# Optimization experiments

Hardware: AMD Instinct MI355X
Metric: run time of the kernel (lower is better)

Reference implementation:

```python
import jax, jax.numpy as jnp
import numpy as np

BATCH = 4
N1 = 131072   # stage-1 voxels (total over batch)
N2 = 32768    # stage-2 (stride-2 downsampled) voxels
D_MODEL = 128
D_INNER = 2 * D_MODEL
D_STATE = 16
D_CONV = 4
DT_RANK = 8   # ceil(d_model / 16)
EPS = 1e-5


def _ln(x, g, b):
    mu = x.mean(-1, keepdims=True)
    v = ((x - mu) ** 2).mean(-1, keepdims=True)
    return (x - mu) * jax.lax.rsqrt(v + EPS) * g + b


def _causal_conv(x, w, b):
    # x: [B,L,Di], w: [Di,K] -> depthwise causal conv1d
    y = jax.lax.conv_general_dilated(
        x.transpose(0, 2, 1), w[:, None, :], (1,), [(D_CONV - 1, 0)],
        dimension_numbers=('NCH', 'OIH', 'NCH'), feature_group_count=D_INNER)
    return y.transpose(0, 2, 1) + b


def _mamba_block(x, ln_g, ln_b, in_w, conv_w, conv_b, xproj_w, dtproj_w, dtproj_b, A_log, Dp, out_w):
    # create_block: LayerNorm -> Mamba mixer (selective scan); returns hidden states
    h = _ln(x, ln_g, ln_b)
    xz = h @ in_w.T                          # [B,L,2*Di]
    xc, z = jnp.split(xz, 2, axis=-1)
    xc = jax.nn.silu(_causal_conv(xc, conv_w, conv_b))
    dbl = xc @ xproj_w.T                     # [B,L,dt_rank+2*d_state]
    dt = jax.nn.softplus(dbl[..., :DT_RANK] @ dtproj_w.T + dtproj_b)  # [B,L,Di]
    Bm = dbl[..., DT_RANK:DT_RANK + D_STATE]
    Cm = dbl[..., DT_RANK + D_STATE:]
    A = -jnp.exp(A_log)                      # [Di,ds]

    def step(hst, inp):
        dt_t, b_t, c_t, u_t = inp            # [B,Di],[B,ds],[B,ds],[B,Di]
        hst = jnp.exp(dt_t[..., None] * A) * hst + (dt_t * u_t)[..., None] * b_t[:, None, :]
        return hst, jnp.einsum('bds,bs->bd', hst, c_t)

    h0 = jnp.zeros((x.shape[0], D_INNER, D_STATE), x.dtype)
    xs = (dt.transpose(1, 0, 2), Bm.transpose(1, 0, 2), Cm.transpose(1, 0, 2), xc.transpose(1, 0, 2))
    _, ys = jax.lax.scan(step, h0, xs)       # ys: [L,B,Di]
    y = ys.transpose(1, 0, 2) + xc * Dp
    y = y * jax.nn.silu(z)
    return y @ out_w.T


def _mamba_params(key):
    ks = jax.random.split(key, 6)
    s = lambda k, sh, sc: jax.random.normal(k, sh, jnp.float32) * sc
    return dict(
        ln_g=jnp.ones((D_MODEL,), jnp.float32), ln_b=jnp.zeros((D_MODEL,), jnp.float32),
        in_w=s(ks[0], (2 * D_INNER, D_MODEL), 0.05),
        conv_w=s(ks[1], (D_INNER, D_CONV), 0.2), conv_b=jnp.zeros((D_INNER,), jnp.float32),
        xproj_w=s(ks[2], (DT_RANK + 2 * D_STATE, D_INNER), 0.05),
        dtproj_w=s(ks[3], (D_INNER, DT_RANK), 0.1), dtproj_b=s(ks[4], (D_INNER,), 0.1),
        A_log=jnp.log(jnp.tile(jnp.arange(1, D_STATE + 1, dtype=jnp.float32), (D_INNER, 1))),
        D=jnp.ones((D_INNER,), jnp.float32),
        out_w=s(ks[5], (D_MODEL, D_INNER), 0.05))


def setup_inputs():
    key = jax.random.key(0)
    k = jax.random.split(key, 10)
    inp = {
        'feats_s1': jax.random.normal(k[0], (N1, D_MODEL), jnp.float32),
        'feats_s2': jax.random.normal(k[1], (N2, D_MODEL), jnp.float32),
        'pos_s1': jax.random.uniform(k[2], (N1, 3), jnp.float32),
        'pos_s2': jax.random.uniform(k[3], (N2, 3), jnp.float32),
        'hilbert_s1': jax.random.randint(k[4], (N1,), 0, 1 << 30, jnp.int32),
        'hilbert_s2': jax.random.randint(k[5], (N2,), 0, 1 << 30, jnp.int32),
        'pe_w': jax.random.normal(k[6], (D_MODEL, 3), jnp.float32) * 0.1,
        'pe_b': jnp.zeros((D_MODEL,), jnp.float32),
        'norm_g': jnp.ones((D_MODEL,), jnp.float32), 'norm_b': jnp.zeros((D_MODEL,), jnp.float32),
        'normb_g': jnp.ones((D_MODEL,), jnp.float32), 'normb_b': jnp.zeros((D_MODEL,), jnp.float32),
    }
    for pref, kk in (('m1_', k[7]), ('m2_', k[8])):
        for n, v in _mamba_params(kk).items():
            inp[pref + n] = v
    return inp


def _forward(feats_s1, feats_s2, pos_s1, pos_s2, pe_w, pe_b, norm_g, norm_b, normb_g, normb_b,
             m1_ln_g, m1_ln_b, m1_in_w, m1_conv_w, m1_conv_b, m1_xproj_w, m1_dtproj_w, m1_dtproj_b, m1_A_log, m1_D, m1_out_w,
             m2_ln_g, m2_ln_b, m2_in_w, m2_conv_w, m2_conv_b, m2_xproj_w, m2_dtproj_w, m2_dtproj_b, m2_A_log, m2_D, m2_out_w,
             hilbert_s1, hilbert_s2):
    L1, L2 = N1 // BATCH, N2 // BATCH
    m1 = (m1_ln_g, m1_ln_b, m1_in_w, m1_conv_w, m1_conv_b, m1_xproj_w, m1_dtproj_w, m1_dtproj_b, m1_A_log, m1_D, m1_out_w)
    m2 = (m2_ln_g, m2_ln_b, m2_in_w, m2_conv_w, m2_conv_b, m2_xproj_w, m2_dtproj_w, m2_dtproj_b, m2_A_log, m2_D, m2_out_w)

    # stage 2: hilbert-order forward scan through mamba_layer1
    f2 = (feats_s2 + pos_s2 @ pe_w.T + pe_b).reshape(BATCH, L2, D_MODEL)
    o2 = jnp.argsort(hilbert_s2.reshape(BATCH, L2), axis=-1)          # inds_curt_to_next
    seq2 = jnp.take_along_axis(f2, o2[..., None], axis=1)
    out2 = _mamba_block(seq2, *m1)
    back2 = jnp.take_along_axis(out2, jnp.argsort(o2, axis=-1)[..., None], axis=1).reshape(N2, D_MODEL)
    out_s2 = _ln(back2, norm_g, norm_b)

    # stage 1: flipped hilbert-order (backward) scan through mamba_layer2
    f1 = (feats_s1 + pos_s1 @ pe_w.T + pe_b).reshape(BATCH, L1, D_MODEL)
    o1 = jnp.argsort(hilbert_s1.reshape(BATCH, L1), axis=-1)
    seq1 = jnp.take_along_axis(f1, o1[..., None], axis=1)[:, ::-1, :]
    out1 = _mamba_block(seq1, *m2)[:, ::-1, :]
    back1 = jnp.take_along_axis(out1, jnp.argsort(o1, axis=-1)[..., None], axis=1).reshape(N1, D_MODEL)
    out_s1 = _ln(back1, normb_g, normb_b)

    return jnp.concatenate([out_s1, out_s2], axis=0)   # [N1+N2, d_model]


def reference(feats_s1, feats_s2, pos_s1, pos_s2, pe_w, pe_b, norm_g, norm_b, normb_g, normb_b,
              m1_ln_g, m1_ln_b, m1_in_w, m1_conv_w, m1_conv_b, m1_xproj_w, m1_dtproj_w, m1_dtproj_b, m1_A_log, m1_D, m1_out_w,
              m2_ln_g, m2_ln_b, m2_in_w, m2_conv_w, m2_conv_b, m2_xproj_w, m2_dtproj_w, m2_dtproj_b, m2_A_log, m2_D, m2_out_w,
              hilbert_s1, hilbert_s2):
    return _forward(feats_s1, feats_s2, pos_s1, pos_s2, pe_w, pe_b, norm_g, norm_b, normb_g, normb_b,
                    m1_ln_g, m1_ln_b, m1_in_w, m1_conv_w, m1_conv_b, m1_xproj_w, m1_dtproj_w, m1_dtproj_b, m1_A_log, m1_D, m1_out_w,
                    m2_ln_g, m2_ln_b, m2_in_w, m2_conv_w, m2_conv_b, m2_xproj_w, m2_dtproj_w, m2_dtproj_b, m2_A_log, m2_D, m2_out_w,
                    hilbert_s1, hilbert_s2)
```

## Files before the change

### kernel.cpp

```cpp
#include <hip/hip_runtime.h>
#include <hip/hip_bf16.h>

#define DEV __device__ __forceinline__

constexpr int BATCH_ = 4;
constexpr int N1_ = 131072;
constexpr int N2_ = 32768;
constexpr int L1_ = N1_ / BATCH_;
constexpr int L2_ = N2_ / BATCH_;
constexpr int DM_ = 128;
constexpr int DI_ = 256;
constexpr int DS_ = 16;
constexpr int DTR_ = 8;
constexpr int TOT_ = N1_ + N2_;

constexpr int TA_ = 32;
constexpr int TAH_ = TA_ + 3;
constexpr int NTILE1_ = L1_ / TA_;
constexpr int NTILE2_ = L2_ / TA_;
constexpr int NTILES_ = 4 * NTILE1_ + 4 * NTILE2_;

constexpr int TS_ = 128;
constexpr int NCH1_ = L1_ / TS_;
constexpr int NCH2_ = L2_ / TS_;
constexpr int NCHUNKS_ = 4 * NCH1_ + 4 * NCH2_;

constexpr int NST_ = 160;

constexpr int PADR_ = 16;
constexpr int SR1_ = L1_ + 2 * PADR_;
constexpr int SR2_ = L2_ + 2 * PADR_;
constexpr int RTOT_ = 4 * SR1_ + 4 * SR2_;

constexpr int IN1_OFF = 0;
constexpr int IN2_OFF = 65536;
constexpr int XP1_OFF = 131072;
constexpr int XP2_OFF = 143360;
constexpr int OW1_OFF = 155648;
constexpr int OW2_OFF = 188416;
constexpr int W16_TOT = 221184;

typedef short short8 __attribute__((ext_vector_type(8)));
typedef float f32x4 __attribute__((ext_vector_type(4)));

struct MP {
  const float* ln_g; const float* ln_b; const float* in_w;
  const float* conv_w; const float* conv_b; const float* xproj_w;
  const float* dtproj_w; const float* dtproj_b; const float* A_log;
  const float* Dp; const float* out_w;
};

DEV float softplusf(float x) {
  return fmaxf(x, 0.f) + __logf(1.f + __expf(-fabsf(x)));
}

DEV unsigned short f2bf(float f) {
  unsigned u = __builtin_bit_cast(unsigned, f);
  u += 0x7fffu + ((u >> 16) & 1u);
  return (unsigned short)(u >> 16);
}
DEV float bf2f(unsigned short s) {
  unsigned u = ((unsigned)s) << 16;
  return __builtin_bit_cast(float, u);
}

DEV void sort_tile_info(int tile, int& seg, int& tis, int& slotbase) {
  if (tile < 128) { seg = tile >> 5; tis = tile & 31; slotbase = seg * L1_; }
  else { seg = 4 + ((tile - 128) >> 3); tis = (tile - 128) & 7; slotbase = N1_ + (seg - 4) * L2_; }
}

__global__ __launch_bounds__(256) void k_prep(
    const float* __restrict__ in_w1, const float* __restrict__ xp1,
    const float* __restrict__ ow1,
    const float* __restrict__ in_w2, const float* __restrict__ xp2,
    const float* __restrict__ ow2,
    unsigned short* __restrict__ w16)
{
  const int i = blockIdx.x * 256 + threadIdx.x;
  if (i >= W16_TOT) return;
  float v;
  if (i < IN2_OFF) v = in_w1[i - IN1_OFF];
  else if (i < XP1_OFF) v = in_w2[i - IN2_OFF];
  else if (i < XP2_OFF) {
    const int j = i - XP1_OFF; const int r = j >> 8;
    v = (r < 40) ? xp1[j] : 0.f;
  } else if (i < OW1_OFF) {
    const int j = i - XP2_OFF; const int r = j >> 8;
    v = (r < 40) ? xp2[j] : 0.f;
  } else if (i < OW2_OFF) v = ow1[i - OW1_OFF];
  else v = ow2[i - OW2_OFF];
  w16[i] = f2bf(v);
}

__global__ __launch_bounds__(256) void k_hist(
    const int* __restrict__ hil1, const int* __restrict__ hil2,
    const unsigned* __restrict__ ksrc, unsigned* __restrict__ histg,
    int shift, int pass0)
{
  const int tile = blockIdx.x;
  int seg, tis, slotbase;
  sort_tile_info(tile, seg, tis, slotbase);
  const int tid = threadIdx.x;
  __shared__ unsigned h[1024];
  #pragma unroll
  for (int i = 0; i < 4; ++i) h[i * 256 + tid] = 0;
  __syncthreads();
  #pragma unroll
  for (int it = 0; it < 4; ++it) {
    const int li = tis * 1024 + it * 256 + tid;
    unsigned k;
    if (pass0) k = (unsigned)(seg < 4 ? hil1[seg * L1_ + li] : hil2[(seg - 4) * L2_ + li]);
    else       k = ksrc[slotbase + li];
    atomicAdd(&h[(k >> shift) & 1023u], 1u);
  }
  __syncthreads();
  #pragma unroll
  for (int i = 0; i < 4; ++i)
    histg[tile * 1024 + i * 256 + tid] = h[i * 256 + tid];
}

__global__ __launch_bounds__(256) void k_scanoff(
    const unsigned* __restrict__ histg, unsigned* __restrict__ offg)
{
  const int seg = blockIdx.x;
  const int ntiles = seg < 4 ? 32 : 8;
  const int tilebase = seg < 4 ? seg * 32 : 128 + (seg - 4) * 8;
  const int tid = threadIdx.x;
  const int d0 = tid * 4;
  unsigned tot[4] = {0, 0, 0, 0};
  for (int t = 0; t < ntiles; ++t) {
    const unsigned* hp = &histg[(size_t)(tilebase + t) * 1024 + d0];
    tot[0] += hp[0]; tot[1] += hp[1]; tot[2] += hp[2]; tot[3] += hp[3];
  }
  unsigned lp[4]; unsigned s = 0;
  #pragma unroll
  for (int j = 0; j < 4; ++j) { lp[j] = s; s += tot[j]; }
  const int lane = tid & 63, wv = tid >> 6;
  unsigned inc = s;
  #pragma unroll
  for (int off = 1; off < 64; off <<= 1) {
    unsigned v = (unsigned)__shfl_up((int)inc, off, 64);
    if (lane >= off) inc += v;
  }
  __shared__ unsigned wsum[4];
  if (lane == 63) wsum[wv] = inc;
  __syncthreads();
  unsigned wbase = 0;
  for (int w = 0; w < 4; ++w) if (w < wv) wbase += wsum[w];
  const unsigned base = wbase + inc - s;
  #pragma unroll
  for (int j = 0; j < 4; ++j) {
    unsigned run = base + lp[j];
    for (int t = 0; t < ntiles; ++t) {
      offg[(size_t)(tilebase + t) * 1024 + d0 + j] = run;
      run += histg[(size_t)(tilebase + t) * 1024 + d0 + j];
    }
  }
}

__global__ __launch_bounds__(256) void k_scatter(
    const int* __restrict__ hil1, const int* __restrict__ hil2,
    const unsigned* __restrict__ ksrc, const int* __restrict__ isrc,
    const unsigned* __restrict__ offg,
    unsigned* __restrict__ kdst, int* __restrict__ idst,
    int* __restrict__ o_all, int shift, int pass0, int last)
{
  const int tile = blockIdx.x;
  int seg, tis, slotbase;
  sort_tile_info(tile, seg, tis, slotbase);
  const int tid = threadIdx.x;
  const int lane = tid & 63, wv = tid >> 6;
  __shared__ unsigned runb[1024];
  __shared__ unsigned wcnt[4 * 1024];
  #pragma unroll
  for (int i = 0; i < 4; ++i) runb[i * 256 + tid] = offg[(size_t)tile * 1024 + i * 256 + tid];
  #pragma unroll
  for (int it = 0; it < 4; ++it) {
    #pragma unroll
    for (int i = 0; i < 16; ++i) wcnt[i * 256 + tid] = 0;
    __syncthreads();
    const int li = tis * 1024 + it * 256 + tid;
    unsigned k; int v;
    if (pass0) {
      k = (unsigned)(seg < 4 ? hil1[seg * L1_ + li] : hil2[(seg - 4) * L2_ + li]);
      v = li;
    } else {
      k = ksrc[slotbase + li]; v = isrc[slotbase + li];
    }
    const unsigned d = (k >> shift) & 1023u;
    unsigned long long m = ~0ull;
    #pragma unroll
    for (int b = 0; b < 10; ++b) {
      const unsigned long long bb = __ballot((int)((d >> b) & 1u));
      m &= ((d >> b) & 1u) ? bb : ~bb;
    }
    const unsigned lrank = (unsigned)__popcll(m & ((1ull << lane) - 1ull));
    wcnt[wv * 1024 + d] = (unsigned)__popcll(m);
    __syncthreads();
    unsigned prior = runb[d];
    for (int w = 0; w < 3; ++w) if (w < wv) prior += wcnt[w * 1024 + d];
    const unsigned pos = prior + lrank;
    if (last) o_all[slotbase + pos] = v;
    else { kdst[slotbase + pos] = k; idst[slotbase + pos] = v; }
    __syncthreads();
    #pragma unroll
    for (int i = 0; i < 4; ++i) {
      const int dd = i * 256 + tid;
      runb[dd] += wcnt[dd] + wcnt[1024 + dd] + wcnt[2048 + dd] + wcnt[3072 + dd];
    }
    __syncthreads();
  }
}

__global__ __launch_bounds__(256) void k_gather(
    const float* __restrict__ feats1, const float* __restrict__ feats2,
    const float* __restrict__ pos1, const float* __restrict__ pos2,
    const float* __restrict__ pe_w, const float* __restrict__ pe_b,
    MP p1, MP p2, const int* __restrict__ o_all,
    unsigned* __restrict__ seq_g)
{
  const int wv = threadIdx.x >> 6, lane = threadIdx.x & 63;
  const int prow = blockIdx.x * 4 + wv;
  if (prow >= RTOT_) return;
  int seg, within;
  if (prow < 4 * SR1_) { seg = prow / SR1_; within = prow - seg * SR1_; }
  else { const int r = prow - 4 * SR1_; seg = 4 + r / SR2_; within = r - (seg - 4) * SR2_; }
  const bool is1 = seg < 4;
  const int b = is1 ? seg : seg - 4;
  const int L = is1 ? L1_ : L2_;
  const int p = within - PADR_;
  unsigned outw = 0;
  if (p >= 0 && p < L) {
    const int slotbase = is1 ? b * L1_ : N1_ + b * L2_;
    const int orig = o_all[slotbase + p];
    const MP P = is1 ? p2 : p1;
    const float* fr = (is1 ? feats1 + (size_t)b * L1_ * DM_
                           : feats2 + (size_t)b * L2_ * DM_) + (size_t)orig * DM_;
    const float* pr = (is1 ? pos1 + (size_t)b * L1_ * 3
                           : pos2 + (size_t)b * L2_ * 3) + (size_t)orig * 3;
    const int c0 = 2 * lane;
    const float2 f = *(const float2*)(fr + c0);
    const float q0 = pr[0], q1 = pr[1], q2 = pr[2];
    float x0 = f.x + q0 * pe_w[c0 * 3 + 0] + q1 * pe_w[c0 * 3 + 1] + q2 * pe_w[c0 * 3 + 2] + pe_b[c0];
    float x1 = f.y + q0 * pe_w[c0 * 3 + 3] + q1 * pe_w[c0 * 3 + 4] + q2 * pe_w[c0 * 3 + 5] + pe_b[c0 + 1];
    float s = x0 + x1, qq = x0 * x0 + x1 * x1;
    #pragma unroll
    for (int off = 32; off; off >>= 1) {
      s += __shfl_xor(s, off, 64);
      qq += __shfl_xor(qq, off, 64);
    }
    const float mu = s * (1.f / 128.f);
    const float rs = rsqrtf(qq * (1.f / 128.f) - mu * mu + 1e-5f);
    const unsigned short o0 = f2bf((x0 - mu) * rs * P.ln_g[c0]     + P.ln_b[c0]);
    const unsigned short o1 = f2bf((x1 - mu) * rs * P.ln_g[c0 + 1] + P.ln_b[c0 + 1]);
    outw = (unsigned)o0 | ((unsigned)o1 << 16);
  }
  seq_g[(size_t)prow * 64 + lane] = outw;
}

constexpr int XB_ = 264;
constexpr int SMEM_A = TAH_ * XB_ * 2;

__global__ __launch_bounds__(256) void k_phaseA(
    MP p1, MP p2,
    const unsigned short* __restrict__ seq_g,
    const unsigned short* __restrict__ w16,
    __hip_bfloat16* __restrict__ xc_g, __hip_bfloat16* __restrict__ z_g,
    float* __restrict__ dbl_g)
{
  const int blk = blockIdx.x;
  bool is1; int b, tile;
  if (blk < 4 * NTILE1_) { is1 = true; b = blk / NTILE1_; tile = blk % NTILE1_; }
  else { const int r = blk - 4 * NTILE1_; is1 = false; b = r / NTILE2_; tile = r % NTILE2_; }
  const int slotbase = is1 ? b * L1_ : N1_ + b * L2_;
  const MP P = is1 ? p2 : p1;
  const unsigned short* iw16 = w16 + (is1 ? IN2_OFF : IN1_OFF);
  const unsigned short* xp16 = w16 + (is1 ? XP2_OFF : XP1_OFF);
  const int segrow0 = is1 ? b * SR1_ : 4 * SR1_ + b * SR2_;
  const unsigned short* seq = seq_g + (size_t)segrow0 * DM_;
  const bool rev = is1;
  const int t0 = tile * TA_;
  const int pstart = rev ? t0 : t0 - 3;
  const int lsh = rev ? 0 : 3;

  __shared__ char smem[SMEM_A];
  unsigned short* xcb16 = (unsigned short*)smem;
  unsigned short* xc16 = xcb16;

  const int tid = threadIdx.x;
  const int lane = tid & 63, wv = tid >> 6;
  const int l15 = lane & 15, quad = lane >> 4;

  #pragma unroll
  for (int mt = 0; mt < 3; ++mt) {
    const int arow = PADR_ + pstart + mt * 16 + l15;
    short8 afr[4];
    #pragma unroll
    for (int t = 0; t < 4; ++t)
      afr[t] = *(const short8*)(seq + (size_t)arow * DM_ + t * 32 + quad * 8);
    #pragma unroll
    for (int nn2 = 0; nn2 < 4; ++nn2) {
      const int ntA = nn2 * 8 + wv;
      const int ntB = nn2 * 8 + 4 + wv;
      f32x4 accA = (f32x4){0.f, 0.f, 0.f, 0.f}, accB = accA;
      #pragma unroll
      for (int t = 0; t < 4; ++t) {
        const short8 bfA = *(const short8*)(iw16 + (size_t)(ntA * 16 + l15) * DM_ + t * 32 + quad * 8);
        const short8 bfB = *(const short8*)(iw16 + (size_t)(ntB * 16 + l15) * DM_ + t * 32 + quad * 8);
        accA = __builtin_amdgcn_mfma_f32_16x16x32_bf16(afr[t], bfA, accA, 0, 0, 0);
        accB = __builtin_amdgcn_mfma_f32_16x16x32_bf16(afr[t], bfB, accB, 0, 0, 0);
      }
      const int row0 = mt * 16 + quad * 4;
      const int colA = ntA * 16 + l15;
      const int colB = ntB * 16 + l15;
      #pragma unroll
      for (int r = 0; r < 4; ++r) {
        const int row = row0 + r;
        if (colA < 256) {
          if (row < TAH_) xcb16[row * XB_ + colA] = f2bf(accA[r]);
        } else {
          const int m = row - lsh;
          if (m >= 0 && m < TA_)
            z_g[(size_t)(slotbase + t0 + m) * DI_ + (colA - 256)] = __float2bfloat16(accA[r]);
        }
        if (colB < 256) {
          if (row < TAH_) xcb16[row * XB_ + colB] = f2bf(accB[r]);
        } else {
          const int m = row - lsh;
          if (m >= 0 && m < TA_)
            z_g[(size_t)(slotbase + t0 + m) * DI_ + (colB - 256)] = __float2bfloat16(accB[r]);
        }
      }
    }
  }
  __syncthreads();
  {
    const int d = tid;
    const float w0 = P.conv_w[d * 4 + 0], w1 = P.conv_w[d * 4 + 1],
                w2 = P.conv_w[d * 4 + 2], w3 = P.conv_w[d * 4 + 3];
    const float cb = P.conv_b[d];
    float x0 = bf2f(xcb16[0 * XB_ + d]), x1 = bf2f(xcb16[1 * XB_ + d]),
          x2 = bf2f(xcb16[2 * XB_ + d]);
    #pragma unroll
    for (int m = 0; m < TA_; ++m) {
      const float x3 = bf2f(xcb16[(m + 3) * XB_ + d]);
      float v;
      if (rev) v = w3 * x0 + w2 * x1 + w1 * x2 + w0 * x3;
      else     v = w0 * x0 + w1 * x1 + w2 * x2 + w3 * x3;
      v += cb;
      v = v * (1.f / (1.f + __expf(-v)));
      const unsigned short vb = f2bf(v);
      xc_g[(size_t)(slotbase + t0 + m) * DI_ + d] = __builtin_bit_cast(__hip_bfloat16, vb);
      xcb16[m * XB_ + d] = vb;
      x0 = x1; x1 = x2; x2 = x3;
    }
  }
  __syncthreads();
  if (wv < 3) {
    f32x4 acc0 = (f32x4){0.f,0.f,0.f,0.f}, acc1 = acc0;
    #pragma unroll
    for (int t = 0; t < 8; ++t) {
      const short8 bfr = *(const short8*)(xp16 + (size_t)(wv * 16 + l15) * DI_ + t * 32 + quad * 8);
      const short8 a0 = *(const short8*)(xc16 + (l15) * XB_ + t * 32 + quad * 8);
      const short8 a1 = *(const short8*)(xc16 + (16 + l15) * XB_ + t * 32 + quad * 8);
      acc0 = __builtin_amdgcn_mfma_f32_16x16x32_bf16(a0, bfr, acc0, 0, 0, 0);
      acc1 = __builtin_amdgcn_mfma_f32_16x16x32_bf16(a1, bfr, acc1, 0, 0, 0);
    }
    const int col = wv * 16 + l15;
    if (col < 40) {
      #pragma unroll
      for (int r = 0; r < 4; ++r) {
        dbl_g[(size_t)(slotbase + t0 + quad * 4 + r) * 40 + col] = acc0[r];
        dbl_g[(size_t)(slotbase + t0 + 16 + quad * 4 + r) * 40 + col] = acc1[r];
      }
    }
  }
}

struct ScanP {
  float Av[DS_]; float A0; bool fast;
  float dtw[DTR_]; float dtb;
};
DEV void load_scanp(const MP& P, int d, ScanP& sp) {
  #pragma unroll
  for (int s = 0; s < DS_; ++s) sp.Av[s] = -__expf(P.A_log[d * DS_ + s]);
  sp.A0 = sp.Av[0];
  bool f = true;
  #pragma unroll
  for (int s = 0; s < DS_; ++s)
    f = f && (fabsf(sp.Av[s] - (float)(s + 1) * sp.A0) <= 1e-3f * (float)(s + 1));
  sp.fast = f;
  #pragma unroll
  for (int r = 0; r < DTR_; ++r) sp.dtw[r] = P.dtproj_w[d * DTR_ + r];
  sp.dtb = P.dtproj_b[d];
}
DEV float dt_from(const float4& q0, const float4& q1, const ScanP& sp) {
  const float dtraw = sp.dtb
      + q0.x*sp.dtw[0] + q0.y*sp.dtw[1] + q0.z*sp.dtw[2] + q0.w*sp.dtw[3]
      + q1.x*sp.dtw[4] + q1.y*sp.dtw[5] + q1.z*sp.dtw[6] + q1.w*sp.dtw[7];
  return softplusf(dtraw);
}

__global__ __launch_bounds__(256) void k_scan1(
    MP p1, MP p2,
    const __hip_bfloat16* __restrict__ xc_g, const float* __restrict__ dbl_g,
    float* __restrict__ hloc, float* __restrict__ sumdt_g)
{
  const int blk = blockIdx.x;
  bool is1; int b, pc;
  if (blk < 4 * NCH1_) { is1 = true; b = blk / NCH1_; pc = blk % NCH1_; }
  else { const int r = blk - 4 * NCH1_; is1 = false; b = r / NCH2_; pc = r % NCH2_; }
  const MP P = is1 ? p2 : p1;
  const int L = is1 ? L1_ : L2_;
  const bool rev = is1;
  const int slotbase = is1 ? b * L1_ : N1_ + b * L2_;
  const int d = threadIdx.x;
  ScanP sp; load_scanp(P, d, sp);
  const unsigned short* xcp = (const unsigned short*)xc_g;
  float h[DS_];
  #pragma unroll
  for (int s = 0; s < DS_; ++s) h[s] = 0.f;
  float sdt = 0.f;
  const int s0 = rev ? (L - (pc + 1) * TS_) : pc * TS_;
  const int dp = rev ? -1 : 1;
  int slot = slotbase + (rev ? (s0 + TS_ - 1) : s0);
  if (sp.fast) {
    const float* dr = dbl_g + (size_t)slot * 40;
    float4 q0 = *(const float4*)dr, q1 = *(const float4*)(dr + 4);
    float4 Bv[4];
    #pragma unroll
    for (int j = 0; j < 4; ++j) Bv[j] = *(const float4*)(dr + 8 + 4 * j);
    float u = bf2f(xcp[(size_t)slot * DI_ + d]);
    for (int i = 0; i < TS_; ++i) {
      const int nslot = (i + 1 < TS_) ? slot + dp : slot;
      const float* nr = dbl_g + (size_t)nslot * 40;
      float4 nq0 = *(const float4*)nr, nq1 = *(const float4*)(nr + 4);
      float4 nB[4];
      #pragma unroll
      for (int j = 0; j < 4; ++j) nB[j] = *(const float4*)(nr + 8 + 4 * j);
      const float nu = bf2f(xcp[(size_t)nslot * DI_ + d]);
      const float dt = dt_from(q0, q1, sp);
      const float du = dt * u;
      sdt += dt;
      const float e1 = __expf(dt * sp.A0);
      const float e2 = e1 * e1, e3 = e2 * e1, e4 = e2 * e2;
      float base = 1.f;
      #pragma unroll
      for (int j = 0; j < 4; ++j) {
        const float m1 = base * e1, m2 = base * e2, m3 = base * e3, m4 = base * e4;
        h[4*j+0] = m1 * h[4*j+0] + du * Bv[j].x;
        h[4*j+1] = m2 * h[4*j+1] + du * Bv[j].y;
        h[4*j+2] = m3 * h[4*j+2] + du * Bv[j].z;
        h[4*j+3] = m4 * h[4*j+3] + du * Bv[j].w;
        base = m4;
      }
      slot = nslot; q0 = nq0; q1 = nq1; u = nu;
      #pragma unroll
      for (int j = 0; j < 4; ++j) Bv[j] = nB[j];
    }
  } else {
    for (int i = 0; i < TS_; ++i) {
      const float* dr = dbl_g + (size_t)slot * 40;
      const float4 q0 = *(const float4*)dr, q1 = *(const float4*)(dr + 4);
      const float dt = dt_from(q0, q1, sp);
      const float u = bf2f(xcp[(size_t)slot * DI_ + d]);
      const float du = dt * u;
      sdt += dt;
      float Bvv[16];
      #pragma unroll
      for (int j = 0; j < 4; ++j) *(float4*)&Bvv[4*j] = *(const float4*)(dr + 8 + 4*j);
      #pragma unroll
      for (int s = 0; s < DS_; ++s)
        h[s] = __expf(dt * sp.Av[s]) * h[s] + du * Bvv[s];
      slot += dp;
    }
  }
  float* hl = hloc + (size_t)blk * DS_ * DI_;
  #pragma unroll
  for (int s = 0; s < DS_; ++s) hl[s * DI_ + d] = h[s];
  sumdt_g[(size_t)blk * DI_ + d] = sdt;
}

__global__ __launch_bounds__(256) void k_scan2(
    MP p1, MP p2, const float* __restrict__ hloc,
    const float* __restrict__ sumdt_g, float* __restrict__ hin)
{
  const int seq = blockIdx.x >> 4;
  const int s = blockIdx.x & 15;
  const bool is1 = seq < 4;
  const int b = is1 ? seq : seq - 4;
  const MP P = is1 ? p2 : p1;
  const int nch = is1 ? NCH1_ : NCH2_;
  const int chbase = is1 ? b * NCH1_ : 4 * NCH1_ + b * NCH2_;
  const int d = threadIdx.x;
  const float A = -__expf(P.A_log[d * DS_ + s]);
  float carry = 0.f;
  for (int pc = 0; pc < nch; ++pc) {
    const size_t idx = (size_t)(chbase + pc);
    const float sdt = sumdt_g[idx * DI_ + d];
    hin[idx * DS_ * DI_ + s * DI_ + d] = carry;
    carry = __expf(A * sdt) * carry + hloc[idx * DS_ * DI_ + s * DI_ + d];
  }
}

__global__ __launch_bounds__(256) void k_scan3(
    MP p1, MP p2,
    const __hip_bfloat16* __restrict__ xc_g, const float* __restrict__ dbl_g,
    const float* __restrict__ hin, __hip_bfloat16* zv_g)
{
  const int blk = blockIdx.x;
  bool is1; int b, pc;
  if (blk < 4 * NCH1_) { is1 = true; b = blk / NCH1_; pc = blk % NCH1_; }
  else { const int r = blk - 4 * NCH1_; is1 = false; b = r / NCH2_; pc = r % NCH2_; }
  const MP P = is1 ? p2 : p1;
  const int L = is1 ? L1_ : L2_;
  const bool rev = is1;
  const int slotbase = is1 ? b * L1_ : N1_ + b * L2_;
  const int d = threadIdx.x;
  ScanP sp; load_scanp(P, d, sp);
  const float Dp = P.Dp[d];
  const unsigned short* xcp = (const unsigned short*)xc_g;
  unsigned short* zvp = (unsigned short*)zv_g;
  float h[DS_];
  const float* hi = hin + (size_t)blk * DS_ * DI_;
  #pragma unroll
  for (int s = 0; s < DS_; ++s) h[s] = hi[s * DI_ + d];
  const int s0 = rev ? (L - (pc + 1) * TS_) : pc * TS_;
  const int dp = rev ? -1 : 1;
  int slot = slotbase + (rev ? (s0 + TS_ - 1) : s0);
  if (sp.fast) {
    const float* dr = dbl_g + (size_t)slot * 40;
    float4 q0 = *(const float4*)dr, q1 = *(const float4*)(dr + 4);
    float4 Bv[4], Cv[4];
    #pragma unroll
    for (int j = 0; j < 4; ++j) {
      Bv[j] = *(const float4*)(dr + 8 + 4 * j);
      Cv[j] = *(const float4*)(dr + 24 + 4 * j);
    }
    float u = bf2f(xcp[(size_t)slot * DI_ + d]);
    float zv = bf2f(zvp[(size_t)slot * DI_ + d]);
    for (int i = 0; i < TS_; ++i) {
      const int nslot = (i + 1 < TS_) ? slot + dp : slot;
      const float* nr = dbl_g + (size_t)nslot * 40;
      float4 nq0 = *(const float4*)nr, nq1 = *(const float4*)(nr + 4);
      float4 nB[4], nC[4];
      #pragma unroll
      for (int j = 0; j < 4; ++j) {
        nB[j] = *(const float4*)(nr + 8 + 4 * j);
        nC[j] = *(const float4*)(nr + 24 + 4 * j);
      }
      const float nu = bf2f(xcp[(size_t)nslot * DI_ + d]);
      const float nz = bf2f(zvp[(size_t)nslot * DI_ + d]);
      const float dt = dt_from(q0, q1, sp);
      const float du = dt * u;
      const float e1 = __expf(dt * sp.A0);
      const float e2 = e1 * e1, e3 = e2 * e1, e4 = e2 * e2;
      float base = 1.f;
      float y = 0.f;
      #pragma unroll
      for (int j = 0; j < 4; ++j) {
        const float m1 = base * e1, m2 = base * e2, m3 = base * e3, m4 = base * e4;
        h[4*j+0] = m1 * h[4*j+0] + du * Bv[j].x;  y += h[4*j+0] * Cv[j].x;
        h[4*j+1] = m2 * h[4*j+1] + du * Bv[j].y;  y += h[4*j+1] * Cv[j].y;
        h[4*j+2] = m3 * h[4*j+2] + du * Bv[j].z;  y += h[4*j+2] * Cv[j].z;
        h[4*j+3] = m4 * h[4*j+3] + du * Bv[j].w;  y += h[4*j+3] * Cv[j].w;
        base = m4;
      }
      const float sg = zv / (1.f + __expf(-zv));
      zvp[(size_t)slot * DI_ + d] = f2bf((y + u * Dp) * sg);
      slot = nslot; q0 = nq0; q1 = nq1; u = nu; zv = nz;
      #pragma unroll
      for (int j = 0; j < 4; ++j) { Bv[j] = nB[j]; Cv[j] = nC[j]; }
    }
  } else {
    for (int i = 0; i < TS_; ++i) {
      const float* dr = dbl_g + (size_t)slot * 40;
      const float4 q0 = *(const float4*)dr, q1 = *(const float4*)(dr + 4);
      const float dt = dt_from(q0, q1, sp);
      const float u = bf2f(xcp[(size_t)slot * DI_ + d]);
      const float zv = bf2f(zvp[(size_t)slot * DI_ + d]);
      const float du = dt * u;
      float Bvv[16], Cvv[16];
      #pragma unroll
      for (int j = 0; j < 4; ++j) {
        *(float4*)&Bvv[4*j] = *(const float4*)(dr + 8 + 4*j);
        *(float4*)&Cvv[4*j] = *(const float4*)(dr + 24 + 4*j);
      }
      float y = 0.f;
      #pragma unroll
      for (int s = 0; s < DS_; ++s) {
        h[s] = __expf(dt * sp.Av[s]) * h[s] + du * Bvv[s];
        y += h[s] * Cvv[s];
      }
      const float sg = zv / (1.f + __expf(-zv));
      zvp[(size_t)slot * DI_ + d] = f2bf((y + u * Dp) * sg);
      slot += dp;
    }
  }
}

constexpr int OB_ = 132;
__global__ __launch_bounds__(256) void k_final(
    const __hip_bfloat16* __restrict__ v_g, const int* __restrict__ o_all,
    const unsigned short* __restrict__ w16,
    const float* __restrict__ norm_g, const float* __restrict__ norm_b,
    const float* __restrict__ normb_g, const float* __restrict__ normb_b,
    float* __restrict__ out)
{
  const int blk = blockIdx.x;
  bool is1; int b, tile;
  if (blk < 4 * NTILE1_) { is1 = true; b = blk / NTILE1_; tile = blk % NTILE1_; }
  else { const int r = blk - 4 * NTILE1_; is1 = false; b = r / NTILE2_; tile = r % NTILE2_; }
  const unsigned short* W = w16 + (is1 ? OW2_OFF : OW1_OFF);
  const float* gg = is1 ? normb_g : norm_g;
  const float* gb = is1 ? normb_b : norm_b;
  const int slotbase = is1 ? b * L1_ : N1_ + b * L2_;
  const int t0 = tile * TA_;
  __shared__ float obuf[TA_ * OB_];
  const int tid = threadIdx.x;
  const int lane = tid & 63, wv = tid >> 6;
  const int l15 = lane & 15, quad = lane >> 4;
  {
    const unsigned short* vp = (const unsigned short*)v_g + (size_t)(slotbase + t0) * DI_;
    f32x4 acc00 = (f32x4){0.f,0.f,0.f,0.f}, acc01 = acc00, acc10 = acc00, acc11 = acc00;
    #pragma unroll
    for (int t = 0; t < 8; ++t) {
      const short8 a0 = *(const short8*)(vp + (size_t)(l15) * DI_ + t * 32 + quad * 8);
      const short8 a1 = *(const short8*)(vp + (size_t)(16 + l15) * DI_ + t * 32 + quad * 8);
      const short8 b0 = *(const short8*)(W + (size_t)((wv) * 16 + l15) * DI_ + t * 32 + quad * 8);
      const short8 b1 = *(const short8*)(W + (size_t)((wv + 4) * 16 + l15) * DI_ + t * 32 + quad * 8);
      acc00 = __builtin_amdgcn_mfma_f32_16x16x32_bf16(a0, b0, acc00, 0, 0, 0);
      acc01 = __builtin_amdgcn_mfma_f32_16x16x32_bf16(a1, b0, acc01, 0, 0, 0);
      acc10 = __builtin_amdgcn_mfma_f32_16x16x32_bf16(a0, b1, acc10, 0, 0, 0);
      acc11 = __builtin_amdgcn_mfma_f32_16x16x32_bf16(a1, b1, acc11, 0, 0, 0);
    }
    const int col0 = wv * 16 + l15;
    const int col1 = (wv + 4) * 16 + l15;
    #pragma unroll
    for (int r = 0; r < 4; ++r) {
      obuf[(quad * 4 + r) * OB_ + col0] = acc00[r];
      obuf[(16 + quad * 4 + r) * OB_ + col0] = acc01[r];
      obuf[(quad * 4 + r) * OB_ + col1] = acc10[r];
      obuf[(16 + quad * 4 + r) * OB_ + col1] = acc11[r];
    }
  }
  __syncthreads();
  {
    for (int m = wv; m < TA_; m += 4) {
      float x0 = obuf[m * OB_ + lane], x1 = obuf[m * OB_ + lane + 64];
      float s = x0 + x1, q = x0 * x0 + x1 * x1;
      #pragma unroll
      for (int off = 32; off; off >>= 1) {
        s += __shfl_xor(s, off, 64);
        q += __shfl_xor(q, off, 64);
      }
      const float mu = s * (1.f / 128.f);
      const float rs = rsqrtf(q * (1.f / 128.f) - mu * mu + 1e-5f);
      const int orig = o_all[slotbase + t0 + m];
      float* orow = out + (size_t)(slotbase + orig) * DM_;
      orow[lane]      = (x0 - mu) * rs * gg[lane]      + gb[lane];
      orow[lane + 64] = (x1 - mu) * rs * gg[lane + 64] + gb[lane + 64];
    }
  }
}

extern "C" void kernel_launch(void* const* d_in, const int* in_sizes, int n_in,
                              void* d_out, int out_size, void* d_ws, size_t ws_size,
                              hipStream_t stream)
{
  (void)in_sizes; (void)n_in; (void)out_size; (void)ws_size;
  const float* feats1 = (const float*)d_in[0];
  const float* feats2 = (const float*)d_in[1];
  const float* pos1   = (const float*)d_in[2];
  const float* pos2   = (const float*)d_in[3];
  const int*   hil1   = (const int*)d_in[4];
  const int*   hil2   = (const int*)d_in[5];
  const float* pe_w   = (const float*)d_in[6];
  const float* pe_b   = (const float*)d_in[7];
  const float* norm_g  = (const float*)d_in[8];
  const float* norm_b  = (const float*)d_in[9];
  const float* normb_g = (const float*)d_in[10];
  const float* normb_b = (const float*)d_in[11];
  MP p1 { (const float*)d_in[12], (const float*)d_in[13], (const float*)d_in[14],
          (const float*)d_in[15], (const float*)d_in[16], (const float*)d_in[17],
          (const float*)d_in[18], (const float*)d_in[19], (const float*)d_in[20],
          (const float*)d_in[21], (const float*)d_in[22] };
  MP p2 { (const float*)d_in[23], (const float*)d_in[24], (const float*)d_in[25],
          (const float*)d_in[26], (const float*)d_in[27], (const float*)d_in[28],
          (const float*)d_in[29], (const float*)d_in[30], (const float*)d_in[31],
          (const float*)d_in[32], (const float*)d_in[33] };

  char* w = (char*)d_ws;
  auto take = [&](size_t bytes) -> char* {
    char* p = w; w += (bytes + 255) & ~(size_t)255; return p;
  };
  int* o_all = (int*)take((size_t)TOT_ * 4);
  unsigned* kA = (unsigned*)take((size_t)TOT_ * 4);
  int* iA = (int*)take((size_t)TOT_ * 4);
  unsigned* kB = (unsigned*)take((size_t)TOT_ * 4);
  int* iB = (int*)take((size_t)TOT_ * 4);
  unsigned* histg = (unsigned*)take((size_t)NST_ * 1024 * 4);
  unsigned* offg  = (unsigned*)take((size_t)NST_ * 1024 * 4);
  __hip_bfloat16* xc = (__hip_bfloat16*)take((size_t)TOT_ * DI_ * 2);
  __hip_bfloat16* vzb = (__hip_bfloat16*)take((size_t)TOT_ * DI_ * 2);
  float* dbl = (float*)take((size_t)TOT_ * 40 * 4);
  float* hloc = (float*)take((size_t)NCHUNKS_ * DS_ * DI_ * 4);
  float* hin  = (float*)take((size_t)NCHUNKS_ * DS_ * DI_ * 4);
  float* sdt  = (float*)take((size_t)NCHUNKS_ * DI_ * 4);
  unsigned short* w16 = (unsigned short*)take((size_t)W16_TOT * 2);
  unsigned* seq = (unsigned*)take((size_t)RTOT_ * DM_ * 2);

  hipLaunchKernelGGL(k_prep, dim3((W16_TOT + 255) / 256), dim3(256), 0, stream,
                     p1.in_w, p1.xproj_w, p1.out_w, p2.in_w, p2.xproj_w, p2.out_w, w16);
  hipLaunchKernelGGL(k_hist, dim3(NST_), dim3(256), 0, stream,
                     hil1, hil2, kB, histg, 0, 1);
  hipLaunchKernelGGL(k_scanoff, dim3(8), dim3(256), 0, stream, histg, offg);
  hipLaunchKernelGGL(k_scatter, dim3(NST_), dim3(256), 0, stream,
                     hil1, hil2, kB, iB, offg, kB, iB, o_all, 0, 1, 0);
  hipLaunchKernelGGL(k_hist, dim3(NST_), dim3(256), 0, stream,
                     hil1, hil2, kB, histg, 10, 0);
  hipLaunchKernelGGL(k_scanoff, dim3(8), dim3(256), 0, stream, histg, offg);
  hipLaunchKernelGGL(k_scatter, dim3(NST_), dim3(256), 0, stream,
                     hil1, hil2, kB, iB, offg, kA, iA, o_all, 10, 0, 0);
  hipLaunchKernelGGL(k_hist, dim3(NST_), dim3(256), 0, stream,
                     hil1, hil2, kA, histg, 20, 0);
  hipLaunchKernelGGL(k_scanoff, dim3(8), dim3(256), 0, stream, histg, offg);
  hipLaunchKernelGGL(k_scatter, dim3(NST_), dim3(256), 0, stream,
                     hil1, hil2, kA, iA, offg, kB, iB, o_all, 20, 0, 1);

  hipLaunchKernelGGL(k_gather, dim3((RTOT_ + 3) / 4), dim3(256), 0, stream,
                     feats1, feats2, pos1, pos2, pe_w, pe_b, p1, p2, o_all, seq);
  hipLaunchKernelGGL(k_phaseA, dim3(NTILES_), dim3(256), 0, stream,
                     p1, p2, (const unsigned short*)seq, w16, xc, vzb, dbl);
  hipLaunchKernelGGL(k_scan1, dim3(NCHUNKS_), dim3(256), 0, stream,
                     p1, p2, xc, dbl, hloc, sdt);
  hipLaunchKernelGGL(k_scan2, dim3(128), dim3(256), 0, stream,
                     p1, p2, hloc, sdt, hin);
  hipLaunchKernelGGL(k_scan3, dim3(NCHUNKS_), dim3(256), 0, stream,
                     p1, p2, xc, dbl, hin, vzb);
  hipLaunchKernelGGL(k_final, dim3(NTILES_), dim3(256), 0, stream,
                     vzb, o_all, w16, norm_g, norm_b, normb_g, normb_b,
                     (float*)d_out);
}
```

Baseline: 989.1 us.

## Stage input tile in LDS and reuse each weight fragment across three row tiles

The in-projection GEMM in phase A now copies the 35-row input tile into shared memory once, zero-pads the tail rows, and loads all A fragments from LDS. The loop order is swapped so each weight fragment loaded from global memory feeds three row-tile MFMAs. Before, the weights were reloaded once per row tile. This cuts repeated global weight traffic to a third, at the cost of extra LDS, a barrier, and more registers held for the A fragments.

Measured after the change: 881.1 us. 10.9% less time.

```diff
diff --git a/kernel.cpp b/kernel.cpp
--- a/kernel.cpp
+++ b/kernel.cpp
@@ -258,8 +258,10 @@
   seq_g[(size_t)prow * 64 + lane] = outw;
 }
 
+constexpr int HB_ = 136;
 constexpr int XB_ = 264;
-constexpr int SMEM_A = TAH_ * XB_ * 2;
+constexpr int OFF_HB16 = TAH_ * XB_ * 2;
+constexpr int SMEM_A = OFF_HB16 + 48 * HB_ * 2;
 
 __global__ __launch_bounds__(256) void k_phaseA(
     MP p1, MP p2,
@@ -285,51 +287,63 @@
 
   __shared__ char smem[SMEM_A];
   unsigned short* xcb16 = (unsigned short*)smem;
+  unsigned short* hb16 = (unsigned short*)(smem + OFF_HB16);
   unsigned short* xc16 = xcb16;
 
   const int tid = threadIdx.x;
   const int lane = tid & 63, wv = tid >> 6;
   const int l15 = lane & 15, quad = lane >> 4;
 
-  #pragma unroll
-  for (int mt = 0; mt < 3; ++mt) {
-    const int arow = PADR_ + pstart + mt * 16 + l15;
-    short8 afr[4];
-    #pragma unroll
-    for (int t = 0; t < 4; ++t)
-      afr[t] = *(const short8*)(seq + (size_t)arow * DM_ + t * 32 + quad * 8);
-    #pragma unroll
-    for (int nn2 = 0; nn2 < 4; ++nn2) {
-      const int ntA = nn2 * 8 + wv;
-      const int ntB = nn2 * 8 + 4 + wv;
-      f32x4 accA = (f32x4){0.f, 0.f, 0.f, 0.f}, accB = accA;
+  {
+    unsigned* hz = (unsigned*)hb16;
+    for (int i = tid; i < 13 * (HB_ / 2); i += 256)
+      hz[TAH_ * (HB_ / 2) + i] = 0;
+    const unsigned short* src = seq + (size_t)(PADR_ + pstart) * DM_;
+    #pragma unroll
+    for (int i = tid; i < TAH_ * 16; i += 256) {
+      const int r = i >> 4, c = (i & 15) * 8;
+      *(uint4*)(hb16 + r * HB_ + c) = *(const uint4*)(src + (size_t)r * DM_ + c);
+    }
+  }
+  __syncthreads();
+  {
+    short8 afr[3][4];
+    #pragma unroll
+    for (int mt = 0; mt < 3; ++mt)
+      #pragma unroll
+      for (int t = 0; t < 4; ++t)
+        afr[mt][t] = *(const short8*)(hb16 + (mt * 16 + l15) * HB_ + t * 32 + quad * 8);
+    for (int nn = 0; nn < 8; ++nn) {
+      const int ntile = nn * 4 + wv;
+      f32x4 acc[3];
+      #pragma unroll
+      for (int mt = 0; mt < 3; ++mt) acc[mt] = (f32x4){0.f, 0.f, 0.f, 0.f};
       #pragma unroll
       for (int t = 0; t < 4; ++t) {
-        const short8 bfA = *(const short8*)(iw16 + (size_t)(ntA * 16 + l15) * DM_ + t * 32 + quad * 8);
-        const short8 bfB = *(const short8*)(iw16 + (size_t)(ntB * 16 + l15) * DM_ + t * 32 + quad * 8);
-        accA = __builtin_amdgcn_mfma_f32_16x16x32_bf16(afr[t], bfA, accA, 0, 0, 0);
-        accB = __builtin_amdgcn_mfma_f32_16x16x32_bf16(afr[t], bfB, accB, 0, 0, 0);
-      }
-      const int row0 = mt * 16 + quad * 4;
-      const int colA = ntA * 16 + l15;
-      const int colB = ntB * 16 + l15;
-      #pragma unroll
-      for (int r = 0; r < 4; ++r) {
-        const int row = row0 + r;
-        if (colA < 256) {
-          if (row < TAH_) xcb16[row * XB_ + colA] = f2bf(accA[r]);
-        } else {
-          const int m = row - lsh;
-          if (m >= 0 && m < TA_)
-            z_g[(size_t)(slotbase + t0 + m) * DI_ + (colA - 256)] = __float2bfloat16(accA[r]);
-        }
-        if (colB < 256) {
-          if (row < TAH_) xcb16[row * XB_ + colB] = f2bf(accB[r]);
-        } else {
-          const int m = row - lsh;
-          if (m >= 0 && m < TA_)
-            z_g[(size_t)(slotbase + t0 + m) * DI_ + (colB - 256)] = __float2bfloat16(accB[r]);
-        }
+        const short8 bfr = *(const short8*)(iw16 + (size_t)(ntile * 16 + l15) * DM_ + t * 32 + quad * 8);
+        #pragma unroll
+        for (int mt = 0; mt < 3; ++mt)
+          acc[mt] = __builtin_amdgcn_mfma_f32_16x16x32_bf16(afr[mt][t], bfr, acc[mt], 0, 0, 0);
+      }
+      const int col = ntile * 16 + l15;
+      if (col < 256) {
+        #pragma unroll
+        for (int mt = 0; mt < 3; ++mt)
+          #pragma unroll
+          for (int r = 0; r < 4; ++r) {
+            const int row = mt * 16 + quad * 4 + r;
+            if (row < TAH_) xcb16[row * XB_ + col] = f2bf(acc[mt][r]);
+          }
+      } else {
+        #pragma unroll
+        for (int mt = 0; mt < 3; ++mt)
+          #pragma unroll
+          for (int r = 0; r < 4; ++r) {
+            const int row = mt * 16 + quad * 4 + r;
+            const int m = row - lsh;
+            if (m >= 0 && m < TA_)
+              z_g[(size_t)(slotbase + t0 + m) * DI_ + (col - 256)] = __float2bfloat16(acc[mt][r]);
+          }
       }
     }
   }
```
